# Optimization experiments

Hardware: AMD Instinct MI355X
Metric: run time of the kernel (lower is better)

Reference implementation:

```python
import jax, jax.numpy as jnp
import numpy as np

VOCAB, EMB, HID = 50000, 256, 512
H = HID // 2            # per-direction hidden size
K = 24                  # tagset size
START, STOP = 22, 23
B, T = 32, 512
NEG = -10000.0


def setup_inputs():
    key = jax.random.key(0)
    ks = jax.random.split(key, 16)
    s = 0.1  # weight scale to keep gates in a sane range
    sentence = jax.random.randint(ks[0], (B, T), 0, VOCAB)
    embedding = jax.random.normal(ks[1], (VOCAB, EMB), jnp.float32)
    w_ih_f = jax.random.normal(ks[2], (4 * H, EMB), jnp.float32) * s
    w_hh_f = jax.random.normal(ks[3], (4 * H, H), jnp.float32) * s
    b_ih_f = jax.random.normal(ks[4], (4 * H,), jnp.float32) * s
    b_hh_f = jax.random.normal(ks[5], (4 * H,), jnp.float32) * s
    w_ih_b = jax.random.normal(ks[6], (4 * H, EMB), jnp.float32) * s
    w_hh_b = jax.random.normal(ks[7], (4 * H, H), jnp.float32) * s
    b_ih_b = jax.random.normal(ks[8], (4 * H,), jnp.float32) * s
    b_hh_b = jax.random.normal(ks[9], (4 * H,), jnp.float32) * s
    w_out = jax.random.normal(ks[10], (K, HID), jnp.float32) * s
    b_out = jax.random.normal(ks[11], (K,), jnp.float32) * s
    transitions = jax.random.normal(ks[12], (K, K), jnp.float32)
    transitions = transitions.at[START, :].set(NEG).at[:, STOP].set(NEG)
    h0 = jax.random.normal(ks[13], (2, B, H), jnp.float32)  # [fwd,bwd] initial h
    c0 = jax.random.normal(ks[14], (2, B, H), jnp.float32)  # [fwd,bwd] initial c
    return {"sentence": sentence, "embedding": embedding,
            "w_ih_f": w_ih_f, "w_hh_f": w_hh_f, "b_ih_f": b_ih_f, "b_hh_f": b_hh_f,
            "w_ih_b": w_ih_b, "w_hh_b": w_hh_b, "b_ih_b": b_ih_b, "b_hh_b": b_hh_b,
            "w_out": w_out, "b_out": b_out, "transitions": transitions,
            "h0": h0, "c0": c0}


def _lstm_dir(x_tbe, w_ih, w_hh, b_ih, b_hh, h0, c0, reverse):
    # x_tbe: [T, B, E]; PyTorch gate order i, f, g, o
    def step(carry, x_t):
        h, c = carry
        gates = x_t @ w_ih.T + b_ih + h @ w_hh.T + b_hh  # [B, 4H]
        i, f, g, o = jnp.split(gates, 4, axis=-1)
        c = jax.nn.sigmoid(f) * c + jax.nn.sigmoid(i) * jnp.tanh(g)
        h = jax.nn.sigmoid(o) * jnp.tanh(c)
        return (h, c), h
    _, hs = jax.lax.scan(step, (h0, c0), x_tbe, reverse=reverse)
    return hs  # [T, B, H]


def _viterbi(feats_tbk, transitions):
    # feats_tbk: [T, B, K]; transitions[next, prev]
    init = jnp.full((B, K), NEG, feats_tbk.dtype).at[:, START].set(0.0)

    def step(fv, feat_t):
        scores = fv[:, None, :] + transitions[None, :, :]  # [B, next, prev]
        bp = jnp.argmax(scores, axis=-1)                   # [B, K]
        fv_new = jnp.max(scores, axis=-1) + feat_t
        return fv_new, bp

    fv, bps = jax.lax.scan(step, init, feats_tbk)  # bps: [T, B, K]
    terminal = fv + transitions[STOP][None, :]
    last_tag = jnp.argmax(terminal, axis=-1)       # [B]
    path_score = jnp.max(terminal, axis=-1)        # [B]

    def back(tag, bp_t):
        prev = jnp.take_along_axis(bp_t, tag[:, None], axis=1)[:, 0]
        return prev, tag
    # process t = T-1 .. 0; carry holds tag at time t, emits it, steps to t-1
    _, path = jax.lax.scan(back, last_tag, bps, reverse=True)  # [T, B]
    return path_score, path.T.astype(jnp.int32)  # [B], [B, T]


def reference(sentence, embedding, w_ih_f, w_hh_f, b_ih_f, b_hh_f,
              w_ih_b, w_hh_b, b_ih_b, b_hh_b, w_out, b_out,
              transitions, h0, c0):
    emb = embedding[sentence]                       # [B, T, EMB]
    x = jnp.transpose(emb, (1, 0, 2))               # [T, B, EMB]
    hf = _lstm_dir(x, w_ih_f, w_hh_f, b_ih_f, b_hh_f, h0[0], c0[0], False)
    hb = _lstm_dir(x, w_ih_b, w_hh_b, b_ih_b, b_hh_b, h0[1], c0[1], True)
    hs = jnp.concatenate([hf, hb], axis=-1)         # [T, B, HID]
    feats = hs @ w_out.T + b_out                    # [T, B, K]
    score, path = _viterbi(feats, transitions)
    return score, path
```

## Files before the change

kernel.cpp:

```cpp
#include <hip/hip_runtime.h>

#define T_LEN 512
#define BATCH 32
#define HDIR  256
#define KTAG  24
#define START_TAG 22
#define STOP_TAG  23
#define NEGV  (-10000.0f)
#define SENTU 0x7FC0DEADu

typedef float vf4 __attribute__((ext_vector_type(4)));

#define XPROJ_OFF   0ull
#define XPROJ_ELEMS (2ull*512*1024*32)
#define FEATS_OFF   (XPROJ_OFF + XPROJ_ELEMS)
#define FEATS_ELEMS (512ull*32*24)
#define HIST_OFF    (FEATS_OFF + FEATS_ELEMS)
#define HIST_ELEMS  (2ull*513*8192)

#define BARRIER_LGKM() asm volatile("s_waitcnt lgkmcnt(0)\n\ts_barrier" ::: "memory")

__device__ __forceinline__ float fsig(float x) {
  return __builtin_amdgcn_rcpf(1.0f + __expf(-x));
}
__device__ __forceinline__ float ftanh(float x) {
  return 2.0f * __builtin_amdgcn_rcpf(1.0f + __expf(-2.0f * x)) - 1.0f;
}
__device__ __forceinline__ unsigned um(unsigned a, unsigned b) { return a < b ? a : b; }

__global__ void k_fill(float* __restrict__ p, int n4) {
  int i = blockIdx.x * blockDim.x + threadIdx.x;
  if (i < n4) {
    float* dst = p + (size_t)i * 4;
    const float sv = __uint_as_float(SENTU);
    vf4 v; v.x = sv; v.y = sv; v.z = sv; v.w = sv;
    asm volatile("global_store_dwordx4 %0, %1, off sc0 sc1"
                 :: "v"(dst), "v"(v) : "memory");
  }
}

__global__ __launch_bounds__(256) void k_xproj(
    const int* __restrict__ sent, const float* __restrict__ emb,
    const float* __restrict__ wf, const float* __restrict__ wb,
    const float* __restrict__ bihf, const float* __restrict__ bhhf,
    const float* __restrict__ bihb, const float* __restrict__ bhhb,
    float* __restrict__ xproj)
{
  __shared__ float As[16][132];
  __shared__ float Bs[16][132];
  __shared__ int sid[128];
  const int tid = threadIdx.x;
  const int m0 = blockIdx.x * 128;
  const int n0 = blockIdx.y * 128;
  const int dir = blockIdx.z;
  const float* __restrict__ W = dir ? wb : wf;
  if (tid < 128) {
    int m = m0 + tid;
    sid[tid] = sent[(m & 31) * 512 + (m >> 5)];
  }
  __syncthreads();
  float acc[8][8];
#pragma unroll
  for (int i = 0; i < 8; ++i)
#pragma unroll
    for (int j = 0; j < 8; ++j) acc[i][j] = 0.f;
  const int r = tid >> 1, qq = tid & 1;
  const int ty = tid >> 4, tx = tid & 15;
  for (int k0 = 0; k0 < 256; k0 += 16) {
    const float* ap = &emb[(size_t)sid[r] * 256 + k0 + qq * 8];
    const float* bp = &W[(size_t)(n0 + r) * 256 + k0 + qq * 8];
    float4 a0 = *(const float4*)ap;
    float4 a1 = *(const float4*)(ap + 4);
    float4 b0 = *(const float4*)bp;
    float4 b1 = *(const float4*)(bp + 4);
    __syncthreads();
    As[qq*8+0][r] = a0.x; As[qq*8+1][r] = a0.y; As[qq*8+2][r] = a0.z; As[qq*8+3][r] = a0.w;
    As[qq*8+4][r] = a1.x; As[qq*8+5][r] = a1.y; As[qq*8+6][r] = a1.z; As[qq*8+7][r] = a1.w;
    Bs[qq*8+0][r] = b0.x; Bs[qq*8+1][r] = b0.y; Bs[qq*8+2][r] = b0.z; Bs[qq*8+3][r] = b0.w;
    Bs[qq*8+4][r] = b1.x; Bs[qq*8+5][r] = b1.y; Bs[qq*8+6][r] = b1.z; Bs[qq*8+7][r] = b1.w;
    __syncthreads();
#pragma unroll
    for (int kk = 0; kk < 16; ++kk) {
      float4 av0 = *(const float4*)&As[kk][ty*8];
      float4 av1 = *(const float4*)&As[kk][ty*8+4];
      float4 bv0 = *(const float4*)&Bs[kk][tx*8];
      float4 bv1 = *(const float4*)&Bs[kk][tx*8+4];
      float am[8] = {av0.x,av0.y,av0.z,av0.w,av1.x,av1.y,av1.z,av1.w};
      float bn[8] = {bv0.x,bv0.y,bv0.z,bv0.w,bv1.x,bv1.y,bv1.z,bv1.w};
#pragma unroll
      for (int i = 0; i < 8; ++i)
#pragma unroll
        for (int j = 0; j < 8; ++j)
          acc[i][j] = fmaf(am[i], bn[j], acc[i][j]);
    }
  }
  const float* bi_p = dir ? bihb : bihf;
  const float* bh_p = dir ? bhhb : bhhf;
  float bias[8];
#pragma unroll
  for (int j = 0; j < 8; ++j) { int n = n0 + tx*8 + j; bias[j] = bi_p[n] + bh_p[n]; }
  const int mb = m0 + ty * 8;
  const int tt = mb >> 5, bb = mb & 31;
#pragma unroll
  for (int j = 0; j < 8; ++j) {
    int n = n0 + tx*8 + j;
    float* dst = &xproj[((((size_t)dir*512 + tt)*1024) + n)*32 + bb];
    float4 s0 = make_float4(acc[0][j]+bias[j], acc[1][j]+bias[j], acc[2][j]+bias[j], acc[3][j]+bias[j]);
    float4 s1 = make_float4(acc[4][j]+bias[j], acc[5][j]+bias[j], acc[6][j]+bias[j], acc[7][j]+bias[j]);
    *(float4*)dst = s0;
    *(float4*)(dst + 4) = s1;
  }
}

__global__ __launch_bounds__(256, 1) void k_lstm(
    const float* __restrict__ whhf, const float* __restrict__ whhb,
    const float* __restrict__ h0, const float* __restrict__ c0,
    const float* __restrict__ xproj, float* __restrict__ hist)
{
  const int wg = blockIdx.x;
  const int dir = wg >> 5;
  const int slice = wg & 31;
  const int tid = threadIdx.x;
  const int rowg = tid >> 5;
  const int bgrp = (tid >> 3) & 3;
  const int kgrp = tid & 7;
  const int jg = slice * 8 + rowg;
  const float* __restrict__ W = dir ? whhb : whhf;
  __shared__ float hl[32 * 256];

  float2 w2[4][16];
#pragma unroll
  for (int g = 0; g < 4; ++g)
#pragma unroll
    for (int kk2 = 0; kk2 < 16; ++kk2)
      w2[g][kk2] = *(const float2*)&W[(size_t)(g*256 + jg)*256 + kgrp*32 + 2*kk2];

  float cc[8];
#pragma unroll
  for (int bi = 0; bi < 8; ++bi)
    cc[bi] = c0[(size_t)(dir*32 + bgrp*8 + bi)*256 + jg];

  const int kk = tid & 31;
  const int base_col = tid & ~31;
  const int kw4 = 4*((tid >> 5) & 7);
  const int rot = (4*kgrp + 2*bgrp) & 31;
  float* const histd = hist + (size_t)dir * 513 * 8192;
  float hnew[8];

  for (int s = 0; s < 512; ++s) {
    const int t = dir ? (511 - s) : s;

    vf4 hv[8];
    if (s == 0) {
#pragma unroll
      for (int q = 0; q < 8; ++q)
#pragma unroll
        for (int bl = 0; bl < 4; ++bl)
          hv[q][bl] = h0[(size_t)(dir*32 + 4*q + bl)*256 + tid];
    } else {
      const float* sp = histd + (size_t)s*8192 + (size_t)tid*4;
      const float* p0 = sp;
      const float* p1 = sp + 1024;
      const float* p2 = sp + 2048;
      const float* p3 = sp + 3072;
      const float* p4 = sp + 4096;
      const float* p5 = sp + 5120;
      const float* p6 = sp + 6144;
      const float* p7 = sp + 7168;
      while (true) {
        asm volatile(
          "global_load_dwordx4 %0, %1, off sc0 sc1\n\t"
          "s_waitcnt vmcnt(0)"
          : "=v"(hv[7]) : "v"(p7) : "memory");
        unsigned z = 0xFFFFFFFFu;
#pragma unroll
        for (int bl = 0; bl < 4; ++bl)
          z = um(z, __float_as_uint(hv[7][bl]) ^ SENTU);
        if (z) break;
        __builtin_amdgcn_s_sleep(1);
      }
      while (true) {
        asm volatile(
          "global_load_dwordx4 %0, %7, off sc0 sc1\n\t"
          "global_load_dwordx4 %1, %8, off sc0 sc1\n\t"
          "global_load_dwordx4 %2, %9, off sc0 sc1\n\t"
          "global_load_dwordx4 %3, %10, off sc0 sc1\n\t"
          "global_load_dwordx4 %4, %11, off sc0 sc1\n\t"
          "global_load_dwordx4 %5, %12, off sc0 sc1\n\t"
          "global_load_dwordx4 %6, %13, off sc0 sc1\n\t"
          "s_waitcnt vmcnt(0)"
          : "=&v"(hv[0]), "=&v"(hv[1]), "=&v"(hv[2]), "=&v"(hv[3]),
            "=&v"(hv[4]), "=&v"(hv[5]), "=&v"(hv[6])
          : "v"(p0), "v"(p1), "v"(p2), "v"(p3),
            "v"(p4), "v"(p5), "v"(p6)
          : "memory");
        unsigned z = 0xFFFFFFFFu;
#pragma unroll
        for (int q = 0; q < 7; ++q)
#pragma unroll
          for (int bl = 0; bl < 4; ++bl)
            z = um(z, __float_as_uint(hv[q][bl]) ^ SENTU);
        if (z) break;
        __builtin_amdgcn_s_sleep(1);
      }
    }

    float xpr[4][8];
    if (kgrp == 0) {
#pragma unroll
      for (int g = 0; g < 4; ++g) {
        const float* xp = &xproj[((((size_t)dir*512 + t)*1024) + g*256 + jg)*32 + bgrp*8];
        float4 x0 = *(const float4*)xp;
        float4 x1 = *(const float4*)(xp + 4);
        xpr[g][0]=x0.x; xpr[g][1]=x0.y; xpr[g][2]=x0.z; xpr[g][3]=x0.w;
        xpr[g][4]=x1.x; xpr[g][5]=x1.y; xpr[g][6]=x1.z; xpr[g][7]=x1.w;
      }
    }

#pragma unroll
    for (int q = 0; q < 8; ++q) {
      const int rwq = (kw4 + 2*((q >> 1) & 3)) & 31;
      const int col = base_col + ((kk + rwq) & 31);
#pragma unroll
      for (int bl = 0; bl < 4; ++bl)
        hl[(4*q + bl)*256 + col] = hv[q][bl];
    }
    BARRIER_LGKM();

    float acc[4][8];
#pragma unroll
    for (int g = 0; g < 4; ++g)
#pragma unroll
      for (int bi = 0; bi < 8; ++bi) acc[g][bi] = 0.f;

    const int hbase = kgrp * 32;
#pragma unroll
    for (int kk2 = 0; kk2 < 16; ++kk2) {
      const int idx = hbase + ((2*kk2 + rot) & 31);
      float2 h2[8];
#pragma unroll
      for (int bi = 0; bi < 8; ++bi)
        h2[bi] = *(const float2*)&hl[(bgrp*8 + bi)*256 + idx];
#pragma unroll
      for (int g = 0; g < 4; ++g)
#pragma unroll
        for (int bi = 0; bi < 8; ++bi) {
          acc[g][bi] = fmaf(w2[g][kk2].x, h2[bi].x, acc[g][bi]);
          acc[g][bi] = fmaf(w2[g][kk2].y, h2[bi].y, acc[g][bi]);
        }
    }

    if (kgrp == 0) {
#pragma unroll
      for (int g = 0; g < 4; ++g)
#pragma unroll
        for (int bi = 0; bi < 8; ++bi) acc[g][bi] += xpr[g][bi];
    }
#pragma unroll
    for (int g = 0; g < 4; ++g)
#pragma unroll
      for (int bi = 0; bi < 8; ++bi) {
        float v = acc[g][bi];
        v += __shfl_xor(v, 1, 64);
        v += __shfl_xor(v, 2, 64);
        v += __shfl_xor(v, 4, 64);
        acc[g][bi] = v;
      }

#pragma unroll
    for (int bi = 0; bi < 8; ++bi) {
      float ig = fsig(acc[0][bi]);
      float fg = fsig(acc[1][bi]);
      float gg = ftanh(acc[2][bi]);
      float og = fsig(acc[3][bi]);
      cc[bi] = fg * cc[bi] + ig * gg;
      hnew[bi] = og * ftanh(cc[bi]);
    }

    if (kgrp == 0) {
      float* dp  = histd + (size_t)(s + 1)*8192 + ((size_t)(2*bgrp)*256 + jg)*4;
      float* dp2 = dp + 1024;
      vf4 s0; s0.x = hnew[0]; s0.y = hnew[1]; s0.z = hnew[2]; s0.w = hnew[3];
      vf4 s1; s1.x = hnew[4]; s1.y = hnew[5]; s1.z = hnew[6]; s1.w = hnew[7];
      asm volatile(
        "global_store_dwordx4 %0, %2, off sc0 sc1\n\t"
        "global_store_dwordx4 %1, %3, off sc0 sc1"
        :: "v"(dp), "v"(dp2), "v"(s0), "v"(s1) : "memory");
    }

    BARRIER_LGKM();
  }
}

__global__ __launch_bounds__(256) void k_feats(
    const float* __restrict__ hist, const float* __restrict__ wout,
    const float* __restrict__ bout, float* __restrict__ feats)
{
  const int t = blockIdx.x;
  const int tid = threadIdx.x;
  __shared__ float hlds[32 * 516];
#pragma unroll
  for (int dir = 0; dir < 2; ++dir) {
    const int slot = dir ? (512 - t) : (t + 1);
    const float* sp = hist + ((size_t)dir*513 + slot)*8192;
#pragma unroll
    for (int q = 0; q < 8; ++q) {
      vf4 v = *(const vf4*)&sp[(size_t)(q*256 + tid)*4];
      float* d = &hlds[(4*q)*516 + dir*256 + tid];
      d[0*516] = v.x; d[1*516] = v.y; d[2*516] = v.z; d[3*516] = v.w;
    }
  }
  __syncthreads();
  const int b = tid >> 3, ks = tid & 7;
#pragma unroll
  for (int kt = 0; kt < 3; ++kt) {
    int k = kt * 8 + ks;
    float acc = bout[k];
    const float* wr = wout + (size_t)k * 512;
#pragma unroll 8
    for (int kk = 0; kk < 512; kk += 4) {
      float4 h4 = *(const float4*)&hlds[b * 516 + kk];
      float4 w4 = *(const float4*)&wr[kk];
      acc += h4.x*w4.x + h4.y*w4.y + h4.z*w4.z + h4.w*w4.w;
    }
    feats[((size_t)t * 32 + b) * 24 + k] = acc;
  }
}

__global__ __launch_bounds__(64) void k_viterbi(
    const float* __restrict__ feats, const float* __restrict__ trans,
    float* __restrict__ out)
{
  const int b = blockIdx.x;
  const int lane = threadIdx.x;
  const int k = lane;
  __shared__ float fvl[2][32];
  __shared__ float pathb[512];
  __shared__ unsigned char bcol[512 * 24];
  float trr[24];
  if (k < 24) {
#pragma unroll
    for (int pv = 0; pv < 24; ++pv) trr[pv] = trans[k * 24 + pv];
  }
  if (k < 32) fvl[0][k] = (k == START_TAG) ? 0.f : NEGV;
  if (k < 32) fvl[1][k] = NEGV;
  __syncthreads();
  float fcur = (k < 24) ? feats[b * 24 + k] : 0.f;
  int q = 0;
  for (int t = 0; t < 512; ++t) {
    float fnext = (t < 511 && k < 24) ? feats[(size_t)(t + 1) * 768 + b * 24 + k] : 0.f;
    float fvp[24];
    {
      const float4* fp4 = (const float4*)&fvl[q][0];
#pragma unroll
      for (int i = 0; i < 6; ++i) {
        float4 v = fp4[i];
        fvp[i*4+0] = v.x; fvp[i*4+1] = v.y; fvp[i*4+2] = v.z; fvp[i*4+3] = v.w;
      }
    }
    float best = -3.4e38f; int bp = 0;
#pragma unroll
    for (int pv = 0; pv < 24; ++pv) {
      float v = fvp[pv] + trr[pv];
      if (v > best) { best = v; bp = pv; }
    }
    if (k < 24) {
      fvl[q ^ 1][k] = best + fcur;
      bcol[t * 24 + k] = (unsigned char)bp;
    }
    fcur = fnext;
    q ^= 1;
    __syncthreads();
  }
  if (lane == 0) {
    float best = -3.4e38f; int bt = 0;
#pragma unroll
    for (int kk = 0; kk < 24; ++kk) {
      float v = fvl[q][kk] + trans[STOP_TAG * 24 + kk];
      if (v > best) { best = v; bt = kk; }
    }
    out[b] = best;
    pathb[511] = (float)bt;
    int tag = bt;
    for (int t = 511; t >= 1; --t) {
      tag = bcol[t * 24 + tag];
      pathb[t - 1] = (float)tag;
    }
  }
  __syncthreads();
#pragma unroll
  for (int it = 0; it < 8; ++it)
    out[32 + (size_t)b * 512 + it * 64 + lane] = pathb[it * 64 + lane];
}

extern "C" void kernel_launch(void* const* d_in, const int* in_sizes, int n_in,
                              void* d_out, int out_size, void* d_ws, size_t ws_size,
                              hipStream_t stream) {
  (void)in_sizes; (void)n_in; (void)out_size; (void)ws_size;
  const int*   sent = (const int*)d_in[0];
  const float* emb  = (const float*)d_in[1];
  const float* wihf = (const float*)d_in[2];
  const float* whhf = (const float*)d_in[3];
  const float* bihf = (const float*)d_in[4];
  const float* bhhf = (const float*)d_in[5];
  const float* wihb = (const float*)d_in[6];
  const float* whhb = (const float*)d_in[7];
  const float* bihb = (const float*)d_in[8];
  const float* bhhb = (const float*)d_in[9];
  const float* wout = (const float*)d_in[10];
  const float* bout = (const float*)d_in[11];
  const float* trans= (const float*)d_in[12];
  const float* h0   = (const float*)d_in[13];
  const float* c0   = (const float*)d_in[14];

  float* ws     = (float*)d_ws;
  float* xproj  = ws + XPROJ_OFF;
  float* feats  = ws + FEATS_OFF;
  float* hist   = ws + HIST_OFF;

  const int n4 = (int)(HIST_ELEMS / 4);
  k_fill<<<(n4 + 255) / 256, 256, 0, stream>>>(hist, n4);
  k_xproj<<<dim3(128, 8, 2), 256, 0, stream>>>(sent, emb, wihf, wihb,
                                               bihf, bhhf, bihb, bhhb, xproj);
  k_lstm<<<64, 256, 0, stream>>>(whhf, whhb, h0, c0, xproj, hist);
  k_feats<<<512, 256, 0, stream>>>(hist, wout, bout, feats);
  k_viterbi<<<32, 64, 0, stream>>>(feats, trans, (float*)d_out);
}
```

Baseline: 4.288 ms.

## Place LSTM workgroups on one XCD and poll via local L2 with escalation

The recurrent LSTM kernel now launches 256 workgroups and keeps only those whose block index modulo 8 is 0 or 1. With round-robin dispatch across the MI355X's chiplets, this likely puts each direction's 32 active workgroups on a single XCD so they share an L2. The spin-wait polls use sc0-only loads that can hit that shared L2 instead of going to system scope, and fall back to sc0 sc1 loads after a bounded number of retries. Stores are issued at both scopes so pollers on either path see the data, and k_feats reads the history with system-coherent loads. The design relies on undocumented dispatch placement; if placement differs, polls stay slow until the escalation kicks in, and the doubled stores add traffic.

```diff
diff --git a/kernel.cpp b/kernel.cpp
--- a/kernel.cpp
+++ b/kernel.cpp
@@ -17,6 +17,8 @@
 #define FEATS_ELEMS (512ull*32*24)
 #define HIST_OFF    (FEATS_OFF + FEATS_ELEMS)
 #define HIST_ELEMS  (2ull*513*8192)
+
+#define ESC_CAP 48u
 
 #define BARRIER_LGKM() asm volatile("s_waitcnt lgkmcnt(0)\n\ts_barrier" ::: "memory")
 
@@ -117,9 +119,10 @@
     const float* __restrict__ h0, const float* __restrict__ c0,
     const float* __restrict__ xproj, float* __restrict__ hist)
 {
-  const int wg = blockIdx.x;
-  const int dir = wg >> 5;
-  const int slice = wg & 31;
+  const int wg8 = blockIdx.x & 7;
+  if (wg8 > 1) return;
+  const int dir = wg8;
+  const int slice = blockIdx.x >> 3;
   const int tid = threadIdx.x;
   const int rowg = tid >> 5;
   const int bgrp = (tid >> 3) & 3;
@@ -146,6 +149,7 @@
   const int rot = (4*kgrp + 2*bgrp) & 31;
   float* const histd = hist + (size_t)dir * 513 * 8192;
   float hnew[8];
+  unsigned esc = 0u;
 
   for (int s = 0; s < 512; ++s) {
     const int t = dir ? (511 - s) : s;
@@ -167,41 +171,73 @@
       const float* p5 = sp + 5120;
       const float* p6 = sp + 6144;
       const float* p7 = sp + 7168;
-      while (true) {
-        asm volatile(
-          "global_load_dwordx4 %0, %1, off sc0 sc1\n\t"
-          "s_waitcnt vmcnt(0)"
-          : "=v"(hv[7]) : "v"(p7) : "memory");
-        unsigned z = 0xFFFFFFFFu;
-#pragma unroll
-        for (int bl = 0; bl < 4; ++bl)
-          z = um(z, __float_as_uint(hv[7][bl]) ^ SENTU);
-        if (z) break;
-        __builtin_amdgcn_s_sleep(1);
+      {
+        unsigned it = 0u;
+        while (true) {
+          if (esc) {
+            asm volatile(
+              "global_load_dwordx4 %0, %1, off sc0 sc1\n\t"
+              "s_waitcnt vmcnt(0)"
+              : "=&v"(hv[7]) : "v"(p7) : "memory");
+          } else {
+            asm volatile(
+              "global_load_dwordx4 %0, %1, off sc0\n\t"
+              "s_waitcnt vmcnt(0)"
+              : "=&v"(hv[7]) : "v"(p7) : "memory");
+          }
+          unsigned z = 0xFFFFFFFFu;
+#pragma unroll
+          for (int bl = 0; bl < 4; ++bl)
+            z = um(z, __float_as_uint(hv[7][bl]) ^ SENTU);
+          if (z) break;
+          if (++it > ESC_CAP) esc = 1u;
+          __builtin_amdgcn_s_sleep(1);
+        }
       }
-      while (true) {
-        asm volatile(
-          "global_load_dwordx4 %0, %7, off sc0 sc1\n\t"
-          "global_load_dwordx4 %1, %8, off sc0 sc1\n\t"
-          "global_load_dwordx4 %2, %9, off sc0 sc1\n\t"
-          "global_load_dwordx4 %3, %10, off sc0 sc1\n\t"
-          "global_load_dwordx4 %4, %11, off sc0 sc1\n\t"
-          "global_load_dwordx4 %5, %12, off sc0 sc1\n\t"
-          "global_load_dwordx4 %6, %13, off sc0 sc1\n\t"
-          "s_waitcnt vmcnt(0)"
-          : "=&v"(hv[0]), "=&v"(hv[1]), "=&v"(hv[2]), "=&v"(hv[3]),
-            "=&v"(hv[4]), "=&v"(hv[5]), "=&v"(hv[6])
-          : "v"(p0), "v"(p1), "v"(p2), "v"(p3),
-            "v"(p4), "v"(p5), "v"(p6)
-          : "memory");
-        unsigned z = 0xFFFFFFFFu;
-#pragma unroll
-        for (int q = 0; q < 7; ++q)
-#pragma unroll
-          for (int bl = 0; bl < 4; ++bl)
-            z = um(z, __float_as_uint(hv[q][bl]) ^ SENTU);
-        if (z) break;
-        __builtin_amdgcn_s_sleep(1);
+      {
+        unsigned it = 0u;
+        while (true) {
+          if (esc) {
+            asm volatile(
+              "global_load_dwordx4 %0, %7, off sc0 sc1\n\t"
+              "global_load_dwordx4 %1, %8, off sc0 sc1\n\t"
+              "global_load_dwordx4 %2, %9, off sc0 sc1\n\t"
+              "global_load_dwordx4 %3, %10, off sc0 sc1\n\t"
+              "global_load_dwordx4 %4, %11, off sc0 sc1\n\t"
+              "global_load_dwordx4 %5, %12, off sc0 sc1\n\t"
+              "global_load_dwordx4 %6, %13, off sc0 sc1\n\t"
+              "s_waitcnt vmcnt(0)"
+              : "=&v"(hv[0]), "=&v"(hv[1]), "=&v"(hv[2]), "=&v"(hv[3]),
+                "=&v"(hv[4]), "=&v"(hv[5]), "=&v"(hv[6])
+              : "v"(p0), "v"(p1), "v"(p2), "v"(p3),
+                "v"(p4), "v"(p5), "v"(p6)
+              : "memory");
+          } else {
+            asm volatile(
+              "global_load_dwordx4 %0, %7, off sc0\n\t"
+              "global_load_dwordx4 %1, %8, off sc0\n\t"
+              "global_load_dwordx4 %2, %9, off sc0\n\t"
+              "global_load_dwordx4 %3, %10, off sc0\n\t"
+              "global_load_dwordx4 %4, %11, off sc0\n\t"
+              "global_load_dwordx4 %5, %12, off sc0\n\t"
+              "global_load_dwordx4 %6, %13, off sc0\n\t"
+              "s_waitcnt vmcnt(0)"
+              : "=&v"(hv[0]), "=&v"(hv[1]), "=&v"(hv[2]), "=&v"(hv[3]),
+                "=&v"(hv[4]), "=&v"(hv[5]), "=&v"(hv[6])
+              : "v"(p0), "v"(p1), "v"(p2), "v"(p3),
+                "v"(p4), "v"(p5), "v"(p6)
+              : "memory");
+          }
+          unsigned z = 0xFFFFFFFFu;
+#pragma unroll
+          for (int q = 0; q < 7; ++q)
+#pragma unroll
+            for (int bl = 0; bl < 4; ++bl)
+              z = um(z, __float_as_uint(hv[q][bl]) ^ SENTU);
+          if (z) break;
+          if (++it > ESC_CAP) esc = 1u;
+          __builtin_amdgcn_s_sleep(1);
+        }
       }
     }
 
@@ -284,7 +320,9 @@
       vf4 s1; s1.x = hnew[4]; s1.y = hnew[5]; s1.z = hnew[6]; s1.w = hnew[7];
       asm volatile(
         "global_store_dwordx4 %0, %2, off sc0 sc1\n\t"
-        "global_store_dwordx4 %1, %3, off sc0 sc1"
+        "global_store_dwordx4 %1, %3, off sc0 sc1\n\t"
+        "global_store_dwordx4 %0, %2, off sc0\n\t"
+        "global_store_dwordx4 %1, %3, off sc0"
         :: "v"(dp), "v"(dp2), "v"(s0), "v"(s1) : "memory");
     }
 
@@ -302,12 +340,27 @@
 #pragma unroll
   for (int dir = 0; dir < 2; ++dir) {
     const int slot = dir ? (512 - t) : (t + 1);
-    const float* sp = hist + ((size_t)dir*513 + slot)*8192;
+    const float* sp = hist + ((size_t)dir*513 + slot)*8192 + (size_t)tid*4;
+    vf4 v[8];
+    asm volatile(
+      "global_load_dwordx4 %0, %8, off sc0 sc1\n\t"
+      "global_load_dwordx4 %1, %9, off sc0 sc1\n\t"
+      "global_load_dwordx4 %2, %10, off sc0 sc1\n\t"
+      "global_load_dwordx4 %3, %11, off sc0 sc1\n\t"
+      "global_load_dwordx4 %4, %12, off sc0 sc1\n\t"
+      "global_load_dwordx4 %5, %13, off sc0 sc1\n\t"
+      "global_load_dwordx4 %6, %14, off sc0 sc1\n\t"
+      "global_load_dwordx4 %7, %15, off sc0 sc1\n\t"
+      "s_waitcnt vmcnt(0)"
+      : "=&v"(v[0]), "=&v"(v[1]), "=&v"(v[2]), "=&v"(v[3]),
+        "=&v"(v[4]), "=&v"(v[5]), "=&v"(v[6]), "=&v"(v[7])
+      : "v"(sp), "v"(sp+1024), "v"(sp+2048), "v"(sp+3072),
+        "v"(sp+4096), "v"(sp+5120), "v"(sp+6144), "v"(sp+7168)
+      : "memory");
 #pragma unroll
     for (int q = 0; q < 8; ++q) {
-      vf4 v = *(const vf4*)&sp[(size_t)(q*256 + tid)*4];
       float* d = &hlds[(4*q)*516 + dir*256 + tid];
-      d[0*516] = v.x; d[1*516] = v.y; d[2*516] = v.z; d[3*516] = v.w;
+      d[0*516] = v[q][0]; d[1*516] = v[q][1]; d[2*516] = v[q][2]; d[3*516] = v[q][3];
     }
   }
   __syncthreads();
@@ -422,7 +475,7 @@
   k_fill<<<(n4 + 255) / 256, 256, 0, stream>>>(hist, n4);
   k_xproj<<<dim3(128, 8, 2), 256, 0, stream>>>(sent, emb, wihf, wihb,
                                                bihf, bhhf, bihb, bhhb, xproj);
-  k_lstm<<<64, 256, 0, stream>>>(whhf, whhb, h0, c0, xproj, hist);
+  k_lstm<<<256, 256, 0, stream>>>(whhf, whhb, h0, c0, xproj, hist);
   k_feats<<<512, 256, 0, stream>>>(hist, wout, bout, feats);
   k_viterbi<<<32, 64, 0, stream>>>(feats, trans, (float*)d_out);
 }
```

Measured after the change: 6.279 ms. +46.4%, slower.

## Fuse input projection into persistent LSTM kernel with sentinel-based dataflow overlap

Applied to the files above, without the earlier changes.

Merges the input-projection GEMM and the recurrent LSTM into one launch. The first 64 blocks run the persistent LSTM, and the remaining blocks compute xproj tiles ordered from both ends of the sequence so that each direction's early timesteps are produced first. The LSTM polls sentinel values in xproj before consuming them, so the recurrence can start before the whole GEMM finishes. The cost is that the whole workspace, including xproj, now has to be sentinel-filled. It also relies on the LSTM blocks staying resident alongside the GEMM blocks, which it encourages with large dynamic shared memory, and adds polling overhead.

```diff
diff --git a/kernel.cpp b/kernel.cpp
--- a/kernel.cpp
+++ b/kernel.cpp
@@ -39,94 +39,105 @@
   }
 }
 
-__global__ __launch_bounds__(256) void k_xproj(
+__global__ __launch_bounds__(256, 1) void k_main(
     const int* __restrict__ sent, const float* __restrict__ emb,
-    const float* __restrict__ wf, const float* __restrict__ wb,
+    const float* __restrict__ wihf, const float* __restrict__ wihb,
     const float* __restrict__ bihf, const float* __restrict__ bhhf,
     const float* __restrict__ bihb, const float* __restrict__ bhhb,
-    float* __restrict__ xproj)
+    const float* __restrict__ whhf, const float* __restrict__ whhb,
+    const float* __restrict__ h0, const float* __restrict__ c0,
+    float* __restrict__ xproj, float* __restrict__ hist)
 {
+  extern __shared__ float dynpad[];
   __shared__ float As[16][132];
   __shared__ float Bs[16][132];
-  __shared__ int sid[128];
+  __shared__ int   sid[128];
+  __shared__ float hl[32 * 256];
+  const int bid = blockIdx.x;
   const int tid = threadIdx.x;
-  const int m0 = blockIdx.x * 128;
-  const int n0 = blockIdx.y * 128;
-  const int dir = blockIdx.z;
-  const float* __restrict__ W = dir ? wb : wf;
-  if (tid < 128) {
-    int m = m0 + tid;
-    sid[tid] = sent[(m & 31) * 512 + (m >> 5)];
-  }
-  __syncthreads();
-  float acc[8][8];
-#pragma unroll
-  for (int i = 0; i < 8; ++i)
-#pragma unroll
-    for (int j = 0; j < 8; ++j) acc[i][j] = 0.f;
-  const int r = tid >> 1, qq = tid & 1;
-  const int ty = tid >> 4, tx = tid & 15;
-  for (int k0 = 0; k0 < 256; k0 += 16) {
-    const float* ap = &emb[(size_t)sid[r] * 256 + k0 + qq * 8];
-    const float* bp = &W[(size_t)(n0 + r) * 256 + k0 + qq * 8];
-    float4 a0 = *(const float4*)ap;
-    float4 a1 = *(const float4*)(ap + 4);
-    float4 b0 = *(const float4*)bp;
-    float4 b1 = *(const float4*)(bp + 4);
+  if (sent == (const int*)0) dynpad[0] = 0.f;
+
+  if (bid >= 64) {
+    const int idx = bid - 64;
+    const int mt_rank = idx >> 4;
+    const int sub = idx & 15;
+    const int y = sub >> 1;
+    const int dir = sub & 1;
+    const int mt = (mt_rank & 1) ? (127 - (mt_rank >> 1)) : (mt_rank >> 1);
+    const int m0 = mt * 128;
+    const int n0 = y * 128;
+    const float* __restrict__ W = dir ? wihb : wihf;
+    if (tid < 128) {
+      int m = m0 + tid;
+      sid[tid] = sent[(m & 31) * 512 + (m >> 5)];
+    }
     __syncthreads();
-    As[qq*8+0][r] = a0.x; As[qq*8+1][r] = a0.y; As[qq*8+2][r] = a0.z; As[qq*8+3][r] = a0.w;
-    As[qq*8+4][r] = a1.x; As[qq*8+5][r] = a1.y; As[qq*8+6][r] = a1.z; As[qq*8+7][r] = a1.w;
-    Bs[qq*8+0][r] = b0.x; Bs[qq*8+1][r] = b0.y; Bs[qq*8+2][r] = b0.z; Bs[qq*8+3][r] = b0.w;
-    Bs[qq*8+4][r] = b1.x; Bs[qq*8+5][r] = b1.y; Bs[qq*8+6][r] = b1.z; Bs[qq*8+7][r] = b1.w;
-    __syncthreads();
-#pragma unroll
-    for (int kk = 0; kk < 16; ++kk) {
-      float4 av0 = *(const float4*)&As[kk][ty*8];
-      float4 av1 = *(const float4*)&As[kk][ty*8+4];
-      float4 bv0 = *(const float4*)&Bs[kk][tx*8];
-      float4 bv1 = *(const float4*)&Bs[kk][tx*8+4];
-      float am[8] = {av0.x,av0.y,av0.z,av0.w,av1.x,av1.y,av1.z,av1.w};
-      float bn[8] = {bv0.x,bv0.y,bv0.z,bv0.w,bv1.x,bv1.y,bv1.z,bv1.w};
-#pragma unroll
-      for (int i = 0; i < 8; ++i)
-#pragma unroll
-        for (int j = 0; j < 8; ++j)
-          acc[i][j] = fmaf(am[i], bn[j], acc[i][j]);
-    }
-  }
-  const float* bi_p = dir ? bihb : bihf;
-  const float* bh_p = dir ? bhhb : bhhf;
-  float bias[8];
-#pragma unroll
-  for (int j = 0; j < 8; ++j) { int n = n0 + tx*8 + j; bias[j] = bi_p[n] + bh_p[n]; }
-  const int mb = m0 + ty * 8;
-  const int tt = mb >> 5, bb = mb & 31;
-#pragma unroll
-  for (int j = 0; j < 8; ++j) {
-    int n = n0 + tx*8 + j;
-    float* dst = &xproj[((((size_t)dir*512 + tt)*1024) + n)*32 + bb];
-    float4 s0 = make_float4(acc[0][j]+bias[j], acc[1][j]+bias[j], acc[2][j]+bias[j], acc[3][j]+bias[j]);
-    float4 s1 = make_float4(acc[4][j]+bias[j], acc[5][j]+bias[j], acc[6][j]+bias[j], acc[7][j]+bias[j]);
-    *(float4*)dst = s0;
-    *(float4*)(dst + 4) = s1;
-  }
-}
-
-__global__ __launch_bounds__(256, 1) void k_lstm(
-    const float* __restrict__ whhf, const float* __restrict__ whhb,
-    const float* __restrict__ h0, const float* __restrict__ c0,
-    const float* __restrict__ xproj, float* __restrict__ hist)
-{
-  const int wg = blockIdx.x;
-  const int dir = wg >> 5;
-  const int slice = wg & 31;
-  const int tid = threadIdx.x;
+    float acc[8][8];
+#pragma unroll
+    for (int i = 0; i < 8; ++i)
+#pragma unroll
+      for (int j = 0; j < 8; ++j) acc[i][j] = 0.f;
+    const int r = tid >> 1, qq = tid & 1;
+    const int ty = tid >> 4, tx = tid & 15;
+    for (int k0 = 0; k0 < 256; k0 += 16) {
+      const float* ap = &emb[(size_t)sid[r] * 256 + k0 + qq * 8];
+      const float* bp = &W[(size_t)(n0 + r) * 256 + k0 + qq * 8];
+      float4 a0 = *(const float4*)ap;
+      float4 a1 = *(const float4*)(ap + 4);
+      float4 b0 = *(const float4*)bp;
+      float4 b1 = *(const float4*)(bp + 4);
+      __syncthreads();
+      As[qq*8+0][r] = a0.x; As[qq*8+1][r] = a0.y; As[qq*8+2][r] = a0.z; As[qq*8+3][r] = a0.w;
+      As[qq*8+4][r] = a1.x; As[qq*8+5][r] = a1.y; As[qq*8+6][r] = a1.z; As[qq*8+7][r] = a1.w;
+      Bs[qq*8+0][r] = b0.x; Bs[qq*8+1][r] = b0.y; Bs[qq*8+2][r] = b0.z; Bs[qq*8+3][r] = b0.w;
+      Bs[qq*8+4][r] = b1.x; Bs[qq*8+5][r] = b1.y; Bs[qq*8+6][r] = b1.z; Bs[qq*8+7][r] = b1.w;
+      __syncthreads();
+#pragma unroll
+      for (int kk = 0; kk < 16; ++kk) {
+        float4 av0 = *(const float4*)&As[kk][ty*8];
+        float4 av1 = *(const float4*)&As[kk][ty*8+4];
+        float4 bv0 = *(const float4*)&Bs[kk][tx*8];
+        float4 bv1 = *(const float4*)&Bs[kk][tx*8+4];
+        float am[8] = {av0.x,av0.y,av0.z,av0.w,av1.x,av1.y,av1.z,av1.w};
+        float bn[8] = {bv0.x,bv0.y,bv0.z,bv0.w,bv1.x,bv1.y,bv1.z,bv1.w};
+#pragma unroll
+        for (int i = 0; i < 8; ++i)
+#pragma unroll
+          for (int j = 0; j < 8; ++j)
+            acc[i][j] = fmaf(am[i], bn[j], acc[i][j]);
+      }
+    }
+    const float* bi_p = dir ? bihb : bihf;
+    const float* bh_p = dir ? bhhb : bhhf;
+    float bias[8];
+#pragma unroll
+    for (int j = 0; j < 8; ++j) { int n = n0 + tx*8 + j; bias[j] = bi_p[n] + bh_p[n]; }
+    const int mb = m0 + ty * 8;
+    const int tt = mb >> 5, bb = mb & 31;
+#pragma unroll
+    for (int j = 0; j < 8; ++j) {
+      int n = n0 + tx*8 + j;
+      float* dst = &xproj[((((size_t)dir*512 + tt)*1024) + n)*32 + bb];
+      vf4 o0, o1;
+      o0[0] = acc[0][j]+bias[j]; o0[1] = acc[1][j]+bias[j];
+      o0[2] = acc[2][j]+bias[j]; o0[3] = acc[3][j]+bias[j];
+      o1[0] = acc[4][j]+bias[j]; o1[1] = acc[5][j]+bias[j];
+      o1[2] = acc[6][j]+bias[j]; o1[3] = acc[7][j]+bias[j];
+      asm volatile(
+        "global_store_dwordx4 %0, %2, off sc0 sc1\n\t"
+        "global_store_dwordx4 %1, %3, off sc0 sc1"
+        :: "v"(dst), "v"(dst + 4), "v"(o0), "v"(o1) : "memory");
+    }
+    return;
+  }
+
+  const int dir = bid >> 5;
+  const int slice = bid & 31;
   const int rowg = tid >> 5;
   const int bgrp = (tid >> 3) & 3;
   const int kgrp = tid & 7;
   const int jg = slice * 8 + rowg;
   const float* __restrict__ W = dir ? whhb : whhf;
-  __shared__ float hl[32 * 256];
 
   float2 w2[4][16];
 #pragma unroll
@@ -171,7 +182,7 @@
         asm volatile(
           "global_load_dwordx4 %0, %1, off sc0 sc1\n\t"
           "s_waitcnt vmcnt(0)"
-          : "=v"(hv[7]) : "v"(p7) : "memory");
+          : "=&v"(hv[7]) : "v"(p7) : "memory");
         unsigned z = 0xFFFFFFFFu;
 #pragma unroll
         for (int bl = 0; bl < 4; ++bl)
@@ -205,16 +216,27 @@
       }
     }
 
-    float xpr[4][8];
+    vf4 xv0, xv1, xv2, xv3, xv4, xv5, xv6, xv7;
+    const float* xb = &xproj[((((size_t)dir*512 + t)*1024) + jg)*32 + bgrp*8];
+    const float* xa0 = xb;             const float* xa1 = xb + 4;
+    const float* xa2 = xb + 8192;      const float* xa3 = xb + 8196;
+    const float* xa4 = xb + 16384;     const float* xa5 = xb + 16388;
+    const float* xa6 = xb + 24576;     const float* xa7 = xb + 24580;
     if (kgrp == 0) {
-#pragma unroll
-      for (int g = 0; g < 4; ++g) {
-        const float* xp = &xproj[((((size_t)dir*512 + t)*1024) + g*256 + jg)*32 + bgrp*8];
-        float4 x0 = *(const float4*)xp;
-        float4 x1 = *(const float4*)(xp + 4);
-        xpr[g][0]=x0.x; xpr[g][1]=x0.y; xpr[g][2]=x0.z; xpr[g][3]=x0.w;
-        xpr[g][4]=x1.x; xpr[g][5]=x1.y; xpr[g][6]=x1.z; xpr[g][7]=x1.w;
-      }
+      asm volatile(
+        "global_load_dwordx4 %0, %8, off sc0 sc1\n\t"
+        "global_load_dwordx4 %1, %9, off sc0 sc1\n\t"
+        "global_load_dwordx4 %2, %10, off sc0 sc1\n\t"
+        "global_load_dwordx4 %3, %11, off sc0 sc1\n\t"
+        "global_load_dwordx4 %4, %12, off sc0 sc1\n\t"
+        "global_load_dwordx4 %5, %13, off sc0 sc1\n\t"
+        "global_load_dwordx4 %6, %14, off sc0 sc1\n\t"
+        "global_load_dwordx4 %7, %15, off sc0 sc1"
+        : "=&v"(xv0), "=&v"(xv1), "=&v"(xv2), "=&v"(xv3),
+          "=&v"(xv4), "=&v"(xv5), "=&v"(xv6), "=&v"(xv7)
+        : "v"(xa0), "v"(xa1), "v"(xa2), "v"(xa3),
+          "v"(xa4), "v"(xa5), "v"(xa6), "v"(xa7)
+        : "memory");
     }
 
 #pragma unroll
@@ -251,10 +273,49 @@
     }
 
     if (kgrp == 0) {
-#pragma unroll
-      for (int g = 0; g < 4; ++g)
-#pragma unroll
-        for (int bi = 0; bi < 8; ++bi) acc[g][bi] += xpr[g][bi];
+      asm volatile("s_waitcnt vmcnt(0)"
+                   : "+v"(xv0), "+v"(xv1), "+v"(xv2), "+v"(xv3),
+                     "+v"(xv4), "+v"(xv5), "+v"(xv6), "+v"(xv7)
+                   :: "memory");
+      while (true) {
+        unsigned z = 0xFFFFFFFFu;
+#pragma unroll
+        for (int bl = 0; bl < 4; ++bl) {
+          z = um(z, __float_as_uint(xv0[bl]) ^ SENTU);
+          z = um(z, __float_as_uint(xv1[bl]) ^ SENTU);
+          z = um(z, __float_as_uint(xv2[bl]) ^ SENTU);
+          z = um(z, __float_as_uint(xv3[bl]) ^ SENTU);
+          z = um(z, __float_as_uint(xv4[bl]) ^ SENTU);
+          z = um(z, __float_as_uint(xv5[bl]) ^ SENTU);
+          z = um(z, __float_as_uint(xv6[bl]) ^ SENTU);
+          z = um(z, __float_as_uint(xv7[bl]) ^ SENTU);
+        }
+        if (z) break;
+        __builtin_amdgcn_s_sleep(1);
+        asm volatile(
+          "global_load_dwordx4 %0, %8, off sc0 sc1\n\t"
+          "global_load_dwordx4 %1, %9, off sc0 sc1\n\t"
+          "global_load_dwordx4 %2, %10, off sc0 sc1\n\t"
+          "global_load_dwordx4 %3, %11, off sc0 sc1\n\t"
+          "global_load_dwordx4 %4, %12, off sc0 sc1\n\t"
+          "global_load_dwordx4 %5, %13, off sc0 sc1\n\t"
+          "global_load_dwordx4 %6, %14, off sc0 sc1\n\t"
+          "global_load_dwordx4 %7, %15, off sc0 sc1\n\t"
+          "s_waitcnt vmcnt(0)"
+          : "=&v"(xv0), "=&v"(xv1), "=&v"(xv2), "=&v"(xv3),
+            "=&v"(xv4), "=&v"(xv5), "=&v"(xv6), "=&v"(xv7)
+          : "v"(xa0), "v"(xa1), "v"(xa2), "v"(xa3),
+            "v"(xa4), "v"(xa5), "v"(xa6), "v"(xa7)
+          : "memory");
+      }
+      acc[0][0]+=xv0[0]; acc[0][1]+=xv0[1]; acc[0][2]+=xv0[2]; acc[0][3]+=xv0[3];
+      acc[0][4]+=xv1[0]; acc[0][5]+=xv1[1]; acc[0][6]+=xv1[2]; acc[0][7]+=xv1[3];
+      acc[1][0]+=xv2[0]; acc[1][1]+=xv2[1]; acc[1][2]+=xv2[2]; acc[1][3]+=xv2[3];
+      acc[1][4]+=xv3[0]; acc[1][5]+=xv3[1]; acc[1][6]+=xv3[2]; acc[1][7]+=xv3[3];
+      acc[2][0]+=xv4[0]; acc[2][1]+=xv4[1]; acc[2][2]+=xv4[2]; acc[2][3]+=xv4[3];
+      acc[2][4]+=xv5[0]; acc[2][5]+=xv5[1]; acc[2][6]+=xv5[2]; acc[2][7]+=xv5[3];
+      acc[3][0]+=xv6[0]; acc[3][1]+=xv6[1]; acc[3][2]+=xv6[2]; acc[3][3]+=xv6[3];
+      acc[3][4]+=xv7[0]; acc[3][5]+=xv7[1]; acc[3][6]+=xv7[2]; acc[3][7]+=xv7[3];
     }
 #pragma unroll
     for (int g = 0; g < 4; ++g)
@@ -418,11 +479,11 @@
   float* feats  = ws + FEATS_OFF;
   float* hist   = ws + HIST_OFF;
 
-  const int n4 = (int)(HIST_ELEMS / 4);
-  k_fill<<<(n4 + 255) / 256, 256, 0, stream>>>(hist, n4);
-  k_xproj<<<dim3(128, 8, 2), 256, 0, stream>>>(sent, emb, wihf, wihb,
-                                               bihf, bhhf, bihb, bhhb, xproj);
-  k_lstm<<<64, 256, 0, stream>>>(whhf, whhb, h0, c0, xproj, hist);
+  const int n4 = (int)((XPROJ_ELEMS + FEATS_ELEMS + HIST_ELEMS) / 4);
+  k_fill<<<(n4 + 255) / 256, 256, 0, stream>>>(ws, n4);
+  k_main<<<2112, 256, 32768, stream>>>(sent, emb, wihf, wihb,
+                                       bihf, bhhf, bihb, bhhb,
+                                       whhf, whhb, h0, c0, xproj, hist);
   k_feats<<<512, 256, 0, stream>>>(hist, wout, bout, feats);
   k_viterbi<<<32, 64, 0, stream>>>(feats, trans, (float*)d_out);
 }
```

Result: slower. 4.387 ms (+2.3%).
